# Optimization experiments

Measured on AMD Instinct MI355X. Metric: run time of the kernel, lower is better.

## Reference

```python
import jax, jax.numpy as jnp
from jax import lax
import numpy as np

GAMMA = 1.0
N, M = 4096, 4096


def setup_inputs() -> dict:
    key = jax.random.key(0)
    D = jax.random.normal(key, (N, M), dtype=jnp.float32)
    return {"D": D}


def reference(D):
    # Faithful translation of the original forward.
    # Step 1: the module overwrites D with exp(-D/gamma); the DP then runs on E.
    E = jnp.exp(-D / GAMMA)  # [N, M]

    # Step 2: hard-min DP (torch.min, despite the "Soft" name):
    #   c[i,j] = E[i,j] + min(c[i-1,j], c[i,j-1], c[i-1,j-1])
    # Row-wise vectorization: within row i, with a[j] = min(prev[j], prev[j-1])
    # (a[0] = prev[0]), the within-row recursion c[j] = E[j] + min(a[j], c[j-1])
    # unrolls to   c[j] = S[j] + cummin(a - S_shift)[j],  S = cumsum(E_row).
    row0 = jnp.cumsum(E[0])  # first row: pure left-to-right accumulation

    def step(prev, e_row):
        a = jnp.minimum(prev, jnp.concatenate([prev[:1], prev[:-1]]))
        S = jnp.cumsum(e_row)
        Sm1 = jnp.concatenate([jnp.zeros((1,), e_row.dtype), S[:-1]])
        c = S + lax.cummin(a - Sm1)
        return c, None

    last_row, _ = lax.scan(step, row0, E[1:])
    cost = last_row[-1]  # acc_cost[N-1, M-1]

    # Step 3: acc_grad. In the original row-major loop, acc_grad[i,j] is still 0
    # when cell (i,j) is processed (all writers come later), so each cell
    # simply (a) subtracts d[i,j]/gamma from itself and (b) adds d[i,j]/gamma to
    # its (i-1,j-1), (i-1,j), (i,j-1) neighbors, with d = exp(-E/gamma).
    # Fully vectorizable as a shifted stencil:
    d = jnp.exp(-E / GAMMA)
    dp = jnp.pad(d, ((0, 1), (0, 1)))  # zero-pad bottom/right for boundary cells
    acc_grad = (dp[1:, 1:] + dp[1:, :-1] + dp[:-1, 1:] - d) / GAMMA

    return cost, acc_grad
```

## Files before the change

kernel.cpp:

```cpp
#include <hip/hip_runtime.h>
#include <math.h>

#define NN 4096
#define STRIPS 32
#define SW 128
#define RING_ROWS 128
#define BATCH 32
#define NBATCH 130
#define PAD 64
#define COLPITCH (NN + 2 * PAD)
#define INFV 1e30f
#define SENTU 0xFFFFFFFFu

__device__ __forceinline__ float dpp_wave_shr1(float x) {
    return __int_as_float(__builtin_amdgcn_update_dpp(
        0, __float_as_int(x), 0x138 , 0xf, 0xf, false));
}

__device__ __forceinline__ float bload(const unsigned* colL, int row, int lane) {
    float v = INFV;
    if (lane < 32 && row < NN) {
        unsigned u = __hip_atomic_load(colL + row, __ATOMIC_RELAXED,
                                       __HIP_MEMORY_SCOPE_AGENT);
        v = __uint_as_float(u);
    }
    return v;
}

__device__ __forceinline__ bool has_sent(float b, int rb, int lane) {
    return __any((lane < 32) && ((rb + lane) < NN) &&
                 (__float_as_uint(b) == SENTU));
}

__device__ __forceinline__ void stageB(const float* Sg, float* ring, int rb,
                                       int lane) {
    #pragma unroll
    for (int k = 0; k < 16; ++k) {
        const int r0 = rb + 2 * k;
        if (r0 < NN) {
            const int slot = r0 & (RING_ROWS - 1);
            const float* gsrc =
                Sg + (size_t)(r0 + (lane >> 5)) * NN + ((lane & 31) << 2);
            __builtin_amdgcn_global_load_lds(
                (const __attribute__((address_space(1))) unsigned*)gsrc,
                (__attribute__((address_space(3))) unsigned*)((char*)ring +
                                                             slot * (SW * 4)),
                16, 0, 0);
        }
    }
}

#define CMP_BARRIER() do {                                          \
    asm volatile("s_waitcnt lgkmcnt(0)" ::: "memory");              \
    __builtin_amdgcn_s_barrier();                                   \
    asm volatile("" ::: "memory");                                  \
} while (0)

#define SUP_BARRIER() do {                                          \
    asm volatile("s_waitcnt vmcnt(0) lgkmcnt(0)" ::: "memory");     \
    __builtin_amdgcn_s_barrier();                                   \
    asm volatile("" ::: "memory");                                  \
} while (0)

template <int DOEXP>
__global__ __launch_bounds__(128, 1) void dtw_dp(const float* __restrict__ S,
                                                 float* __restrict__ cost_out,
                                                 unsigned* __restrict__ colbuf) {
    __shared__ float ring[RING_ROWS * SW];
    __shared__ float inbox[2][32];
    __shared__ float outbox[2][32];
    __shared__ float outdummy[64];

    const int tid = threadIdx.x;
    const int lane = tid & 63;
    const int b = blockIdx.x;
    const int g = ((b & 7) << 2) | (b >> 3);

    const float* Sg = S + g * SW;
    const unsigned* colL = colbuf + (size_t)(g - 1) * COLPITCH + PAD;
    unsigned* colM = colbuf + (size_t)g * COLPITCH + PAD;

    if (tid < 64) {
        {
            const float4 z = make_float4(0.f, 0.f, 0.f, 0.f);
            float4* r4 = reinterpret_cast<float4*>(&ring[64 * SW]);
            #pragma unroll
            for (int i = 0; i < 32; ++i) r4[i * 64 + lane] = z;
        }
        CMP_BARRIER();

        const bool lane0 = (lane == 0);
        const int ostep = (lane == 63) ? 1 : 0;
        float cur0 = INFV, cur1 = INFV;
        float l1s = INFV, l2s = INFV;
        float bprevc = INFV;
        float save = 0.f;

        for (int n = 0; n < NBATCH; ++n) {
            const int tb = n << 5;
            const float binb = inbox[n & 1][lane & 31];

            float2 rv[BATCH];
            #pragma unroll
            for (int s = 0; s < BATCH; ++s) {
                const int r = tb + s - lane;
                rv[s] = *reinterpret_cast<const float2*>(
                    &ring[(r & (RING_ROWS - 1)) * SW + 2 * lane]);
            }
            __builtin_amdgcn_sched_barrier(0);

            float* obp = (lane == 63) ? &outbox[n & 1][0] : &outdummy[lane];
            float pbc = INFV;
            #pragma unroll
            for (int s = 0; s < BATCH; ++s) {
                float e0, e1;
                if (DOEXP) { e0 = __expf(-rv[s].x); e1 = __expf(-rv[s].y); }
                else       { e0 = rv[s].x;          e1 = rv[s].y; }

                float bcur;
                if (g == 0)
                    bcur = (n == 0 && s == 0) ? 0.f : INFV;
                else
                    bcur = __int_as_float(
                        __builtin_amdgcn_readlane(__float_as_int(binb), s));
                const float bpv =
                    (g == 0) ? INFV : ((s == 0) ? bprevc : pbc);

                const float L1 = lane0 ? bcur : l1s;
                const float L2 = lane0 ? bpv : l2s;
                const float m0 = fminf(fminf(L1, cur0), L2);
                const float c0 = e0 + m0;
                const float c1 = e1 + fminf(c0, fminf(cur0, cur1));
                *obp = c1;
                obp += ostep;
                const float sh = dpp_wave_shr1(c1);
                l2s = l1s; l1s = sh;
                cur0 = c0; cur1 = c1;
                pbc = bcur;
                if (s == 30) save = c1;
            }
            bprevc = pbc;
            CMP_BARRIER();
        }
        if (g == STRIPS - 1 && lane == 63) cost_out[0] = save;
    } else {
        stageB(Sg, ring, 0, lane);
        float qv = INFV;
        if (g > 0) {
            qv = bload(colL, lane, lane);
            while (has_sent(qv, 0, lane)) qv = bload(colL, lane, lane);
            if (lane < 32) inbox[0][lane] = qv;
            qv = bload(colL, 32 + lane, lane);
        }
        SUP_BARRIER();

        for (int n = 0; n < NBATCH; ++n) {
            const int tb = n << 5;
            if (g > 0) {
                const int vb = tb + 32;
                while (has_sent(qv, vb, lane)) qv = bload(colL, vb + lane, lane);
                if (lane < 32) inbox[(n + 1) & 1][lane] = qv;
                qv = bload(colL, tb + 64 + lane, lane);
            }
            if (n > 0 && lane < 32) {
                const int row = ((n - 1) << 5) - 63 + lane;
                __hip_atomic_store(colM + row,
                                   __float_as_uint(outbox[(n - 1) & 1][lane]),
                                   __ATOMIC_RELAXED, __HIP_MEMORY_SCOPE_AGENT);
            }
            stageB(Sg, ring, tb + 32, lane);
            SUP_BARRIER();
        }
        if (lane < 32) {
            const int row = ((NBATCH - 1) << 5) - 63 + lane;
            __hip_atomic_store(colM + row,
                               __float_as_uint(outbox[(NBATCH - 1) & 1][lane]),
                               __ATOMIC_RELAXED, __HIP_MEMORY_SCOPE_AGENT);
        }
    }
}

__global__ __launch_bounds__(256) void exp_pre(const float* __restrict__ D,
                                               float* __restrict__ E) {
    const int n4 = NN * NN / 4;
    for (int i = blockIdx.x * 256 + threadIdx.x; i < n4; i += 2048 * 256) {
        float4 v = reinterpret_cast<const float4*>(D)[i];
        v.x = __expf(-v.x); v.y = __expf(-v.y);
        v.z = __expf(-v.z); v.w = __expf(-v.w);
        reinterpret_cast<float4*>(E)[i] = v;
    }
}

__device__ __forceinline__ float dfun(float x) { return __expf(-__expf(-x)); }

__global__ __launch_bounds__(256) void dtw_grad_kernel(const float* __restrict__ D,
                                                       float* __restrict__ G) {
    const int idx = blockIdx.x * 256 + threadIdx.x;
    const int i = idx >> 10;
    const int j = (idx & 1023) << 2;
    if (i >= NN) return;

    const float* row0 = D + (size_t)i * NN + j;
    const bool hasR = (i + 1) < NN;
    const bool hasC = (j + 4) < NN;

    const float4 r0 = *reinterpret_cast<const float4*>(row0);
    float4 r1 = make_float4(0.f, 0.f, 0.f, 0.f);
    if (hasR) r1 = *reinterpret_cast<const float4*>(row0 + NN);
    const float s0 = hasC ? row0[4] : 0.f;
    const float s1 = (hasR && hasC) ? row0[NN + 4] : 0.f;

    const float a0 = dfun(r0.x), a1 = dfun(r0.y), a2 = dfun(r0.z), a3 = dfun(r0.w);
    const float a4 = hasC ? dfun(s0) : 0.f;
    const float b0 = hasR ? dfun(r1.x) : 0.f;
    const float b1 = hasR ? dfun(r1.y) : 0.f;
    const float b2 = hasR ? dfun(r1.z) : 0.f;
    const float b3 = hasR ? dfun(r1.w) : 0.f;
    const float b4 = (hasR && hasC) ? dfun(s1) : 0.f;

    float* go = G + (size_t)i * NN + j;
    go[0] = b1 + b0 + a1 - a0;
    go[1] = b2 + b1 + a2 - a1;
    go[2] = b3 + b2 + a3 - a2;
    go[3] = b4 + b3 + a4 - a3;
}

extern "C" void kernel_launch(void* const* d_in, const int* in_sizes, int n_in,
                              void* d_out, int out_size, void* d_ws, size_t ws_size,
                              hipStream_t stream) {
    (void)in_sizes; (void)n_in; (void)out_size;
    const float* D = (const float*)d_in[0];
    float* out = (float*)d_out;

    const size_t colbytes = (size_t)STRIPS * COLPITCH * sizeof(unsigned);
    const size_t ebytes = (size_t)NN * NN * sizeof(float);

    float* E = nullptr;
    unsigned* colbuf;
    if (ws_size >= ebytes + colbytes) {
        E = (float*)d_ws;
        colbuf = (unsigned*)((char*)d_ws + ebytes);
    } else if (ws_size >= colbytes) {
        colbuf = (unsigned*)d_ws;
    } else {
        colbuf = (unsigned*)(out + 1);
    }

    hipMemsetAsync(colbuf, 0xFF, colbytes, stream);
    if (E) {
        exp_pre<<<2048, 256, 0, stream>>>(D, E);
        dtw_dp<0><<<STRIPS, 128, 0, stream>>>(E, out, colbuf);
    } else {
        dtw_dp<1><<<STRIPS, 128, 0, stream>>>(D, out, colbuf);
    }
    dtw_grad_kernel<<<dim3((NN * (NN / 4)) / 256), dim3(256), 0, stream>>>(D, out + 1);
}
```

Baseline: 523.6 us.

## Double-buffer DP ring reads, deepen prefetch, and fuse exp with gradient kernel

The LDS ring grows to 256 rows. The compute wave now loads the next batch of ring values into a second register array while it processes the current batch. The supplier wave prefetches two batches ahead and waits on a partial vmcnt instead of draining all loads, and out-of-range loads are clamped rather than branched around. The exp precompute and gradient stencil are merged into one kernel, so D is read once for both outputs. These changes aim to hide LDS and global latency on the serial DP critical path and to save a full pass over memory, at the cost of more registers and LDS and fragile hand-tuned waitcnt values.

```diff
diff --git a/kernel.cpp b/kernel.cpp
--- a/kernel.cpp
+++ b/kernel.cpp
@@ -4,7 +4,8 @@
 #define NN 4096
 #define STRIPS 32
 #define SW 128
-#define RING_ROWS 128
+#define RING_ROWS 256
+#define RINGB (RING_ROWS * SW * 4)
 #define BATCH 32
 #define NBATCH 130
 #define PAD 64
@@ -19,8 +20,9 @@
 
 __device__ __forceinline__ float bload(const unsigned* colL, int row, int lane) {
     float v = INFV;
-    if (lane < 32 && row < NN) {
-        unsigned u = __hip_atomic_load(colL + row, __ATOMIC_RELAXED,
+    const int rowc = (row < NN) ? row : (NN - 1);
+    if (lane < 32) {
+        unsigned u = __hip_atomic_load(colL + rowc, __ATOMIC_RELAXED,
                                        __HIP_MEMORY_SCOPE_AGENT);
         v = __uint_as_float(u);
     }
@@ -37,30 +39,17 @@
     #pragma unroll
     for (int k = 0; k < 16; ++k) {
         const int r0 = rb + 2 * k;
-        if (r0 < NN) {
-            const int slot = r0 & (RING_ROWS - 1);
-            const float* gsrc =
-                Sg + (size_t)(r0 + (lane >> 5)) * NN + ((lane & 31) << 2);
-            __builtin_amdgcn_global_load_lds(
-                (const __attribute__((address_space(1))) unsigned*)gsrc,
-                (__attribute__((address_space(3))) unsigned*)((char*)ring +
-                                                             slot * (SW * 4)),
-                16, 0, 0);
-        }
-    }
-}
-
-#define CMP_BARRIER() do {                                          \
-    asm volatile("s_waitcnt lgkmcnt(0)" ::: "memory");              \
-    __builtin_amdgcn_s_barrier();                                   \
-    asm volatile("" ::: "memory");                                  \
-} while (0)
-
-#define SUP_BARRIER() do {                                          \
-    asm volatile("s_waitcnt vmcnt(0) lgkmcnt(0)" ::: "memory");     \
-    __builtin_amdgcn_s_barrier();                                   \
-    asm volatile("" ::: "memory");                                  \
-} while (0)
+        const int r0c = (r0 < NN - 1) ? r0 : (NN - 2);
+        const int slot = r0 & (RING_ROWS - 1);
+        const float* gsrc =
+            Sg + (size_t)(r0c + (lane >> 5)) * NN + ((lane & 31) << 2);
+        __builtin_amdgcn_global_load_lds(
+            (const __attribute__((address_space(1))) unsigned*)gsrc,
+            (__attribute__((address_space(3))) unsigned*)((char*)ring +
+                                                         slot * (SW * 4)),
+            16, 0, 0);
+    }
+}
 
 template <int DOEXP>
 __global__ __launch_bounds__(128, 1) void dtw_dp(const float* __restrict__ S,
@@ -83,11 +72,12 @@
     if (tid < 64) {
         {
             const float4 z = make_float4(0.f, 0.f, 0.f, 0.f);
-            float4* r4 = reinterpret_cast<float4*>(&ring[64 * SW]);
+            float4* r4 = reinterpret_cast<float4*>(&ring[192 * SW]);
             #pragma unroll
             for (int i = 0; i < 32; ++i) r4[i * 64 + lane] = z;
         }
-        CMP_BARRIER();
+        asm volatile("s_waitcnt lgkmcnt(0)" ::: "memory");
+        __builtin_amdgcn_s_barrier();
 
         const bool lane0 = (lane == 0);
         const int ostep = (lane == 63) ? 1 : 0;
@@ -96,71 +86,86 @@
         float bprevc = INFV;
         float save = 0.f;
 
-        for (int n = 0; n < NBATCH; ++n) {
-            const int tb = n << 5;
-            const float binb = inbox[n & 1][lane & 31];
-
-            float2 rv[BATCH];
-            #pragma unroll
-            for (int s = 0; s < BATCH; ++s) {
-                const int r = tb + s - lane;
-                rv[s] = *reinterpret_cast<const float2*>(
-                    &ring[(r & (RING_ROWS - 1)) * SW + 2 * lane]);
-            }
-            __builtin_amdgcn_sched_barrier(0);
-
-            float* obp = (lane == 63) ? &outbox[n & 1][0] : &outdummy[lane];
-            float pbc = INFV;
-            #pragma unroll
-            for (int s = 0; s < BATCH; ++s) {
-                float e0, e1;
-                if (DOEXP) { e0 = __expf(-rv[s].x); e1 = __expf(-rv[s].y); }
-                else       { e0 = rv[s].x;          e1 = rv[s].y; }
-
-                float bcur;
-                if (g == 0)
-                    bcur = (n == 0 && s == 0) ? 0.f : INFV;
-                else
-                    bcur = __int_as_float(
-                        __builtin_amdgcn_readlane(__float_as_int(binb), s));
-                const float bpv =
-                    (g == 0) ? INFV : ((s == 0) ? bprevc : pbc);
-
-                const float L1 = lane0 ? bcur : l1s;
-                const float L2 = lane0 ? bpv : l2s;
-                const float m0 = fminf(fminf(L1, cur0), L2);
-                const float c0 = e0 + m0;
-                const float c1 = e1 + fminf(c0, fminf(cur0, cur1));
-                *obp = c1;
-                obp += ostep;
-                const float sh = dpp_wave_shr1(c1);
-                l2s = l1s; l1s = sh;
-                cur0 = c0; cur1 = c1;
-                pbc = bcur;
-                if (s == 30) save = c1;
-            }
-            bprevc = pbc;
-            CMP_BARRIER();
-        }
+        unsigned caddr = ((unsigned)((0 - lane) & (RING_ROWS - 1)) << 9) |
+                         ((unsigned)lane << 3);
+
+        float2 rvA[BATCH], rvB[BATCH];
+        #pragma unroll
+        for (int s = 0; s < BATCH; ++s)
+            rvA[s] = *reinterpret_cast<const float2*>(
+                (const char*)ring + ((caddr + s * 512) & (RINGB - 1)));
+
+#define CSTEP(CUR, NXT, NIDX) do {                                            \
+        const int n_ = (NIDX);                                                \
+        const float binb = inbox[n_ & 1][lane & 31];                          \
+        _Pragma("unroll")                                                     \
+        for (int s = 0; s < BATCH; ++s)                                       \
+            NXT[s] = *reinterpret_cast<const float2*>(                        \
+                (const char*)ring +                                           \
+                ((caddr + 16384u + (unsigned)(s * 512)) & (RINGB - 1)));      \
+        __builtin_amdgcn_sched_barrier(0);                                    \
+        float* obp = (lane == 63) ? &outbox[n_ & 1][0] : &outdummy[lane];     \
+        float pbc = INFV;                                                     \
+        _Pragma("unroll")                                                     \
+        for (int s = 0; s < BATCH; ++s) {                                     \
+            float e0, e1;                                                     \
+            if (DOEXP) { e0 = __expf(-CUR[s].x); e1 = __expf(-CUR[s].y); }    \
+            else       { e0 = CUR[s].x;          e1 = CUR[s].y; }             \
+            float bcur;                                                       \
+            if (g == 0)                                                       \
+                bcur = (n_ == 0 && s == 0) ? 0.f : INFV;                      \
+            else                                                              \
+                bcur = __int_as_float(                                        \
+                    __builtin_amdgcn_readlane(__float_as_int(binb), s));      \
+            const float bpv =                                                 \
+                (g == 0) ? INFV : ((s == 0) ? bprevc : pbc);                  \
+            const float L1 = lane0 ? bcur : l1s;                              \
+            const float L2 = lane0 ? bpv : l2s;                               \
+            const float m0 = fminf(fminf(L1, cur0), L2);                      \
+            const float c0 = e0 + m0;                                         \
+            const float c1 = e1 + fminf(c0, fminf(cur0, cur1));               \
+            *obp = c1;                                                        \
+            obp += ostep;                                                     \
+            const float sh = dpp_wave_shr1(c1);                               \
+            l2s = l1s; l1s = sh;                                              \
+            cur0 = c0; cur1 = c1;                                             \
+            pbc = bcur;                                                       \
+            if (s == 30) save = c1;                                           \
+        }                                                                     \
+        bprevc = pbc;                                                         \
+        caddr = (caddr + 16384u) & (RINGB - 1);                               \
+        asm volatile("s_waitcnt lgkmcnt(0)" ::: "memory");                    \
+        __builtin_amdgcn_s_barrier();                                         \
+    } while (0)
+
+        for (int i = 0; i < NBATCH / 2; ++i) {
+            CSTEP(rvA, rvB, 2 * i);
+            CSTEP(rvB, rvA, 2 * i + 1);
+        }
+#undef CSTEP
+
         if (g == STRIPS - 1 && lane == 63) cost_out[0] = save;
     } else {
         stageB(Sg, ring, 0, lane);
+        stageB(Sg, ring, 32, lane);
         float qv = INFV;
         if (g > 0) {
-            qv = bload(colL, lane, lane);
-            while (has_sent(qv, 0, lane)) qv = bload(colL, lane, lane);
+            qv = bload(colL, lane & 31, lane);
+            while (has_sent(qv, 0, lane)) qv = bload(colL, lane & 31, lane);
             if (lane < 32) inbox[0][lane] = qv;
-            qv = bload(colL, 32 + lane, lane);
-        }
-        SUP_BARRIER();
+            qv = bload(colL, 32 + (lane & 31), lane);
+        }
+        asm volatile("s_waitcnt vmcnt(0) lgkmcnt(0)" ::: "memory");
+        __builtin_amdgcn_s_barrier();
 
         for (int n = 0; n < NBATCH; ++n) {
             const int tb = n << 5;
             if (g > 0) {
                 const int vb = tb + 32;
-                while (has_sent(qv, vb, lane)) qv = bload(colL, vb + lane, lane);
+                while (has_sent(qv, vb, lane))
+                    qv = bload(colL, vb + (lane & 31), lane);
                 if (lane < 32) inbox[(n + 1) & 1][lane] = qv;
-                qv = bload(colL, tb + 64 + lane, lane);
+                qv = bload(colL, tb + 64 + (lane & 31), lane);
             }
             if (n > 0 && lane < 32) {
                 const int row = ((n - 1) << 5) - 63 + lane;
@@ -168,8 +173,13 @@
                                    __float_as_uint(outbox[(n - 1) & 1][lane]),
                                    __ATOMIC_RELAXED, __HIP_MEMORY_SCOPE_AGENT);
             }
-            stageB(Sg, ring, tb + 32, lane);
-            SUP_BARRIER();
+            stageB(Sg, ring, tb + 64, lane);
+            __builtin_amdgcn_sched_barrier(0);
+            if (g > 0) asm volatile("s_waitcnt vmcnt(18)" ::: "memory");
+            else       asm volatile("s_waitcnt vmcnt(17)" ::: "memory");
+            __builtin_amdgcn_sched_barrier(0);
+            asm volatile("s_waitcnt lgkmcnt(0)" ::: "memory");
+            __builtin_amdgcn_s_barrier();
         }
         if (lane < 32) {
             const int row = ((NBATCH - 1) << 5) - 63 + lane;
@@ -180,15 +190,43 @@
     }
 }
 
-__global__ __launch_bounds__(256) void exp_pre(const float* __restrict__ D,
-                                               float* __restrict__ E) {
-    const int n4 = NN * NN / 4;
-    for (int i = blockIdx.x * 256 + threadIdx.x; i < n4; i += 2048 * 256) {
-        float4 v = reinterpret_cast<const float4*>(D)[i];
-        v.x = __expf(-v.x); v.y = __expf(-v.y);
-        v.z = __expf(-v.z); v.w = __expf(-v.w);
-        reinterpret_cast<float4*>(E)[i] = v;
-    }
+__global__ __launch_bounds__(256) void eg_kernel(const float* __restrict__ D,
+                                                 float* __restrict__ E,
+                                                 float* __restrict__ G) {
+    const int idx = blockIdx.x * 256 + threadIdx.x;
+    const int i = idx >> 10;
+    const int j = (idx & 1023) << 2;
+    if (i >= NN) return;
+
+    const float* row0 = D + (size_t)i * NN + j;
+    const bool hasR = (i + 1) < NN;
+    const bool hasC = (j + 4) < NN;
+
+    const float4 r0 = *reinterpret_cast<const float4*>(row0);
+    float4 r1 = make_float4(0.f, 0.f, 0.f, 0.f);
+    if (hasR) r1 = *reinterpret_cast<const float4*>(row0 + NN);
+    const float s0 = hasC ? row0[4] : 0.f;
+    const float s1 = (hasR && hasC) ? row0[NN + 4] : 0.f;
+
+    const float ex0 = __expf(-r0.x), ex1 = __expf(-r0.y);
+    const float ex2 = __expf(-r0.z), ex3 = __expf(-r0.w);
+    *reinterpret_cast<float4*>(E + (size_t)i * NN + j) =
+        make_float4(ex0, ex1, ex2, ex3);
+
+    const float a0 = __expf(-ex0), a1 = __expf(-ex1);
+    const float a2 = __expf(-ex2), a3 = __expf(-ex3);
+    const float a4 = hasC ? __expf(-__expf(-s0)) : 0.f;
+    const float b0 = hasR ? __expf(-__expf(-r1.x)) : 0.f;
+    const float b1 = hasR ? __expf(-__expf(-r1.y)) : 0.f;
+    const float b2 = hasR ? __expf(-__expf(-r1.z)) : 0.f;
+    const float b3 = hasR ? __expf(-__expf(-r1.w)) : 0.f;
+    const float b4 = (hasR && hasC) ? __expf(-__expf(-s1)) : 0.f;
+
+    float* go = G + (size_t)i * NN + j;
+    go[0] = b1 + b0 + a1 - a0;
+    go[1] = b2 + b1 + a2 - a1;
+    go[2] = b3 + b2 + a3 - a2;
+    go[3] = b4 + b3 + a4 - a3;
 }
 
 __device__ __forceinline__ float dfun(float x) { return __expf(-__expf(-x)); }
@@ -234,24 +272,19 @@
 
     const size_t colbytes = (size_t)STRIPS * COLPITCH * sizeof(unsigned);
     const size_t ebytes = (size_t)NN * NN * sizeof(float);
-
-    float* E = nullptr;
-    unsigned* colbuf;
+    const int gblocks = (NN * (NN / 4)) / 256;
+
     if (ws_size >= ebytes + colbytes) {
-        E = (float*)d_ws;
-        colbuf = (unsigned*)((char*)d_ws + ebytes);
-    } else if (ws_size >= colbytes) {
-        colbuf = (unsigned*)d_ws;
-    } else {
-        colbuf = (unsigned*)(out + 1);
-    }
-
-    hipMemsetAsync(colbuf, 0xFF, colbytes, stream);
-    if (E) {
-        exp_pre<<<2048, 256, 0, stream>>>(D, E);
+        float* E = (float*)d_ws;
+        unsigned* colbuf = (unsigned*)((char*)d_ws + ebytes);
+        hipMemsetAsync(colbuf, 0xFF, colbytes, stream);
+        eg_kernel<<<gblocks, 256, 0, stream>>>(D, E, out + 1);
         dtw_dp<0><<<STRIPS, 128, 0, stream>>>(E, out, colbuf);
     } else {
+        unsigned* colbuf = (ws_size >= colbytes) ? (unsigned*)d_ws
+                                                 : (unsigned*)(out + 1);
+        hipMemsetAsync(colbuf, 0xFF, colbytes, stream);
         dtw_dp<1><<<STRIPS, 128, 0, stream>>>(D, out, colbuf);
-    }
-    dtw_grad_kernel<<<dim3((NN * (NN / 4)) / 256), dim3(256), 0, stream>>>(D, out + 1);
-}
+        dtw_grad_kernel<<<gblocks, 256, 0, stream>>>(D, out + 1);
+    }
+}
```

Result: faster. 465.8 us (-11.0%).
